# Optimization experiments

Hardware: AMD Instinct MI355X
Metric: run time of the kernel (lower is better)

## Reference

```python
import jax, jax.numpy as jnp
import numpy as np

B, T, D = 4096, 200, 64
N_USERS, N_ITEMS = 100000, 100000


def _linear_init(k, out_dim, in_dim):
    kw, kb = jax.random.split(k)
    lim = 1.0 / np.sqrt(in_dim)
    w = jax.random.uniform(kw, (out_dim, in_dim), minval=-lim, maxval=lim, dtype=jnp.float32)
    b = jax.random.uniform(kb, (out_dim,), minval=-lim, maxval=lim, dtype=jnp.float32)
    return w, b


def setup_inputs() -> dict:
    key = jax.random.key(0)
    ks = jax.random.split(key, 16)
    gru_w_ih, gru_b_ih = _linear_init(ks[0], 3 * D, D)   # torch GRU gate order: r, z, n
    gru_w_hh, gru_b_hh = _linear_init(ks[1], 3 * D, D)
    attn_w, attn_b = _linear_init(ks[2], D, D)
    wr_w, wr_b = _linear_init(ks[3], D, 2 * D)
    wz_w, wz_b = _linear_init(ks[4], D, 2 * D)
    wh_w, wh_b = _linear_init(ks[5], D, 2 * D)
    aux_w, aux_b = _linear_init(ks[6], 1, D)
    item_emb = jax.random.normal(ks[7], (N_ITEMS + 1, D), dtype=jnp.float32)
    user_bias = jax.random.normal(ks[8], (N_USERS, 1), dtype=jnp.float32) * 0.01
    item_bias = jax.random.normal(ks[9], (N_ITEMS, 1), dtype=jnp.float32) * 0.01
    u_idx = jax.random.randint(ks[10], (B,), 0, N_USERS)
    i_idx = jax.random.randint(ks[11], (B,), 0, N_ITEMS)
    seq = jax.random.randint(ks[12], (B, T), 0, N_ITEMS + 1)
    return dict(u_idx=u_idx, i_idx=i_idx, seq=seq,
                item_emb=item_emb, user_bias=user_bias, item_bias=item_bias,
                gru_w_ih=gru_w_ih, gru_b_ih=gru_b_ih, gru_w_hh=gru_w_hh, gru_b_hh=gru_b_hh,
                attn_w=attn_w, attn_b=attn_b,
                wr_w=wr_w, wr_b=wr_b, wz_w=wz_w, wz_b=wz_b, wh_w=wh_w, wh_b=wh_b,
                aux_w=aux_w, aux_b=aux_b)


def _gru(seq_emb, w_ih, b_ih, w_hh, b_hh):
    # seq_emb: [B, T, D]. Precompute input projections for all timesteps.
    x_proj = jnp.einsum('btd,gd->btg', seq_emb, w_ih) + b_ih  # [B, T, 3D]
    x_proj = jnp.transpose(x_proj, (1, 0, 2))                 # [T, B, 3D]
    h0 = jnp.zeros((seq_emb.shape[0], D), dtype=seq_emb.dtype)

    def step(h, xp):
        gh = h @ w_hh.T + b_hh
        xr, xz, xn = jnp.split(xp, 3, axis=-1)
        hr, hz, hn = jnp.split(gh, 3, axis=-1)
        r = jax.nn.sigmoid(xr + hr)
        z = jax.nn.sigmoid(xz + hz)
        n = jnp.tanh(xn + r * hn)
        h_new = (1.0 - z) * n + z * h
        return h_new, h_new

    _, hs = jax.lax.scan(step, h0, x_proj)
    return jnp.transpose(hs, (1, 0, 2))  # [B, T, D]


def _augru(seq_emb, attn_w_t, wr_w, wr_b, wz_w, wz_b, wh_w, wh_b):
    # Split each [D, 2D] weight into x-part and h-part (input was concat([x, h])).
    wr_x, wr_h = wr_w[:, :D], wr_w[:, D:]
    wz_x, wz_h = wz_w[:, :D], wz_w[:, D:]
    wh_x, wh_h = wh_w[:, :D], wh_w[:, D:]
    xr = jnp.einsum('btd,hd->bth', seq_emb, wr_x) + wr_b  # [B, T, D]
    xz = jnp.einsum('btd,hd->bth', seq_emb, wz_x) + wz_b
    xh = jnp.einsum('btd,hd->bth', seq_emb, wh_x) + wh_b
    h0 = jnp.zeros((seq_emb.shape[0], D), dtype=seq_emb.dtype)
    inputs = (jnp.transpose(xr, (1, 0, 2)), jnp.transpose(xz, (1, 0, 2)),
              jnp.transpose(xh, (1, 0, 2)), attn_w_t.T)  # [T,B,D]x3, [T,B]

    def step(h, inp):
        xr_t, xz_t, xh_t, a_t = inp
        r = jax.nn.sigmoid(xr_t + h @ wr_h.T)
        z = jax.nn.sigmoid(xz_t + h @ wz_h.T)
        h_hat = jnp.tanh(xh_t + (r * h) @ wh_h.T)
        z = a_t[:, None] * z
        h_new = (1.0 - z) * h + z * h_hat
        return h_new, None

    h_final, _ = jax.lax.scan(step, h0, inputs)
    return h_final  # [B, D]


def reference(u_idx, i_idx, seq, item_emb, user_bias, item_bias,
              gru_w_ih, gru_b_ih, gru_w_hh, gru_b_hh, attn_w, attn_b,
              wr_w, wr_b, wz_w, wz_b, wh_w, wh_b, aux_w, aux_b):
    fm1 = user_bias[u_idx] + item_bias[i_idx]          # [B, 1]
    target_emb = item_emb[i_idx]                       # [B, D]
    seq_emb = item_emb[seq]                            # [B, T, D]

    gru_out = _gru(seq_emb, gru_w_ih, gru_b_ih, gru_w_hh, gru_b_hh)  # [B, T, D]

    target_proj = target_emb @ attn_w.T + attn_b       # [B, D]
    attn_scores = jnp.einsum('btd,bd->bt', gru_out, target_proj)
    attn_weights = jax.nn.sigmoid(attn_scores)         # [B, T]

    attn_vec = _augru(seq_emb, attn_weights, wr_w, wr_b, wz_w, wz_b, wh_w, wh_b)  # [B, D]

    aux_logits = (gru_out[:, -1, :] @ aux_w.T + aux_b)[:, 0]  # [B]
    return (fm1, attn_vec, aux_logits)
```

## Files before the change

kernel.cpp:

```cpp
#include <hip/hip_runtime.h>

typedef __bf16 bf16x8 __attribute__((ext_vector_type(8)));
typedef float f32x4 __attribute__((ext_vector_type(4)));

#define T_LEN 200
#define NB 4096

__device__ __forceinline__ f32x4 mfma16(bf16x8 a, bf16x8 b, f32x4 c) {
    return __builtin_amdgcn_mfma_f32_16x16x32_bf16(a, b, c, 0, 0, 0);
}
__device__ __forceinline__ float sigf(float x) {
    return __builtin_amdgcn_rcpf(1.0f + __expf(-x));
}
__device__ __forceinline__ float tanh_fast(float x) {
    return 1.0f - 2.0f * __builtin_amdgcn_rcpf(__expf(2.0f * x) + 1.0f);
}

__device__ __forceinline__ unsigned packRNE2(float a, float b) {
    unsigned ha = (unsigned)__builtin_bit_cast(unsigned short, (__bf16)a);
    unsigned hb = (unsigned)__builtin_bit_cast(unsigned short, (__bf16)b);
    return ha | (hb << 16);
}
__device__ __forceinline__ void publish_hi(unsigned short* hp, float v) {
    __bf16 h = (__bf16)v;
    *hp = __builtin_bit_cast(unsigned short, h);
}

struct Frag { bf16x8 hi, lo; };
__device__ __forceinline__ Frag make_frag(f32x4 a, f32x4 b) {
    Frag f;
    #pragma unroll
    for (int j = 0; j < 4; j++) {
        float v = a[j]; __bf16 h = (__bf16)v;
        f.hi[j] = h; f.lo[j] = (__bf16)(v - (float)h);
    }
    #pragma unroll
    for (int j = 0; j < 4; j++) {
        float v = b[j]; __bf16 h = (__bf16)v;
        f.hi[4 + j] = h; f.lo[4 + j] = (__bf16)(v - (float)h);
    }
    return f;
}
__device__ __forceinline__ bf16x8 load_w(const float* p) {
    f32x4 a = *(const f32x4*)p, b = *(const f32x4*)(p + 4);
    bf16x8 w;
    #pragma unroll
    for (int j = 0; j < 4; j++) { w[j] = (__bf16)a[j]; w[4 + j] = (__bf16)b[j]; }
    return w;
}

__global__ __launch_bounds__(512, 2)
void dien_fused(const int* __restrict__ u_idx, const int* __restrict__ i_idx,
                const int* __restrict__ seq, const float* __restrict__ item_emb,
                const float* __restrict__ user_bias, const float* __restrict__ item_bias,
                const float* __restrict__ gw_ih, const float* __restrict__ gb_ih,
                const float* __restrict__ gw_hh, const float* __restrict__ gb_hh,
                const float* __restrict__ attn_w, const float* __restrict__ attn_b,
                const float* __restrict__ wr_w, const float* __restrict__ wr_b,
                const float* __restrict__ wz_w, const float* __restrict__ wz_b,
                const float* __restrict__ wh_w, const float* __restrict__ wh_b,
                const float* __restrict__ aux_w, const float* __restrict__ aux_b,
                float* __restrict__ out)
{
    __shared__ int sSeq[16][T_LEN];
    __shared__ __align__(16) float sTP[16][64];
    __shared__ __align__(16) unsigned short sHGhi[16][72];
    __shared__ __align__(16) unsigned short sHAhi[16][72];
    __shared__ __align__(16) unsigned short sRHhi[16][72];
    __shared__ __align__(16) unsigned short sXhi[16][72];
    __shared__ float sScore[2][16];
    __shared__ float sParts[16][4];

    const int tid  = threadIdx.x;
    const int wave = tid >> 6;
    const int lane = tid & 63;
    const int c    = lane & 15;
    const int q    = lane >> 4;
    const bool isG = (wave < 4);
    const int wg   = wave & 3;
    const int dglob = wg * 16 + c;
    const int row0 = blockIdx.x * 16;

    for (int i = tid; i < 16 * T_LEN; i += 512) {
        int b = i / T_LEN, t = i - b * T_LEN;
        sSeq[b][t] = seq[(row0 + b) * T_LEN + t];
    }

    if (tid < 16) {
        int b = row0 + tid;
        out[b] = user_bias[u_idx[b]] + item_bias[i_idx[b]];
    }

    if (tid < 256) {
        int b  = tid >> 4;
        int d0 = (tid & 15) * 4;
        const float* erow = item_emb + (long)i_idx[row0 + b] * 64;
        float e[64];
        #pragma unroll
        for (int k4 = 0; k4 < 16; k4++) {
            f32x4 v = *(const f32x4*)(erow + k4 * 4);
            #pragma unroll
            for (int j = 0; j < 4; j++) e[k4 * 4 + j] = v[j];
        }
        #pragma unroll
        for (int dd = 0; dd < 4; dd++) {
            int d = d0 + dd;
            const float* wrow = attn_w + d * 64;
            float s = attn_b[d];
            #pragma unroll
            for (int k4 = 0; k4 < 16; k4++) {
                f32x4 wv = *(const f32x4*)(wrow + k4 * 4);
                #pragma unroll
                for (int j = 0; j < 4; j++) s += e[k4 * 4 + j] * wv[j];
            }
            sTP[b][d] = s;
        }
    }

    for (int i = tid; i < 16 * 72; i += 512) sHAhi[0][i] = 0;
    const int xrow = wg * 4 + (lane >> 4);
    const int xch  = lane & 15;
    if (isG) {
        const float* p = item_emb + (long)seq[(row0 + xrow) * T_LEN + 0] * 64 + xch * 4;
        f32x4 v = *(const f32x4*)p;
        *(uint2*)&sXhi[xrow][xch * 4] =
            make_uint2(packRNE2(v[0], v[1]), packRNE2(v[2], v[3]));
    }
    __syncthreads();

    bf16x8 W[12];
    if (isG) {
        #pragma unroll
        for (int g = 0; g < 3; g++)
            #pragma unroll
            for (int s = 0; s < 2; s++) {
                W[g * 2 + s]     = load_w(gw_ih + (g * 64 + dglob) * 64 + s * 32 + q * 8);
                W[6 + g * 2 + s] = load_w(gw_hh + (g * 64 + dglob) * 64 + s * 32 + q * 8);
            }
    } else {
        #pragma unroll
        for (int s = 0; s < 2; s++) {
            const int fo = dglob * 128 + s * 32 + q * 8;
            W[0 + s]  = load_w(wr_w + fo);
            W[2 + s]  = load_w(wr_w + fo + 64);
            W[4 + s]  = load_w(wz_w + fo);
            W[6 + s]  = load_w(wz_w + fo + 64);
            W[8 + s]  = load_w(wh_w + fo);
            W[10 + s] = load_w(wh_w + fo + 64);
        }
    }

    float bA, bB, bC, bD;
    if (isG) {
        bA = gb_ih[dglob] + gb_hh[dglob];
        bB = gb_ih[64 + dglob] + gb_hh[64 + dglob];
        bC = gb_ih[128 + dglob];
        bD = gb_hh[128 + dglob];
    } else {
        bA = wr_b[dglob];
        bB = wz_b[dglob];
        bC = wh_b[dglob];
        bD = 0.0f;
    }
    const float auxwc = aux_w[dglob];

    Frag tpB0, tpB1;
    if (isG) {
        tpB0 = make_frag(*(const f32x4*)&sTP[c][q * 8], *(const f32x4*)&sTP[c][q * 8 + 4]);
        tpB1 = make_frag(*(const f32x4*)&sTP[c][32 + q * 8], *(const f32x4*)&sTP[c][32 + q * 8 + 4]);
    }

    float hst[4] = {0.f, 0.f, 0.f, 0.f};
    bf16x8 fr0, fr1;
    #pragma unroll
    for (int j = 0; j < 8; j++) { fr0[j] = (__bf16)0.f; fr1[j] = (__bf16)0.f; }
    f32x4 aAH = {0.f, 0.f, 0.f, 0.f};
    float z_c[4] = {0.f, 0.f, 0.f, 0.f};

    for (int t = 0; t < T_LEN; t++) {
        f32x4 xg;
        f32x4 aAR, aAZ;

        bf16x8 x0 = *(const bf16x8*)&sXhi[c][q * 8];
        bf16x8 x1 = *(const bf16x8*)&sXhi[c][32 + q * 8];

        if (isG) {
            int tn = (t + 1 < T_LEN) ? t + 1 : t;
            xg = *(const f32x4*)(item_emb + (long)sSeq[xrow][tn] * 64 + xch * 4);

            f32x4 accR = {bA, bA, bA, bA};
            accR = mfma16(x0, W[0], accR); accR = mfma16(x1, W[1], accR);
            accR = mfma16(fr0, W[6], accR); accR = mfma16(fr1, W[7], accR);
            f32x4 accZ = {bB, bB, bB, bB};
            accZ = mfma16(x0, W[2], accZ); accZ = mfma16(x1, W[3], accZ);
            accZ = mfma16(fr0, W[8], accZ); accZ = mfma16(fr1, W[9], accZ);
            f32x4 accNX = {bC, bC, bC, bC};
            accNX = mfma16(x0, W[4], accNX); accNX = mfma16(x1, W[5], accNX);
            f32x4 accNH = {bD, bD, bD, bD};
            accNH = mfma16(fr0, W[10], accNH); accNH = mfma16(fr1, W[11], accNH);

            #pragma unroll
            for (int i = 0; i < 4; i++) {
                float r = sigf(accR[i]);
                float z = sigf(accZ[i]);
                float n = tanh_fast(accNX[i] + r * accNH[i]);
                float hn = n + z * (hst[i] - n);
                hst[i] = hn;
                publish_hi(&sHGhi[q * 4 + i][dglob], hn);
            }
        } else {
            if (t > 0) {
                bf16x8 rh0 = *(const bf16x8*)&sRHhi[c][q * 8];
                bf16x8 rh1 = *(const bf16x8*)&sRHhi[c][32 + q * 8];
                aAH = mfma16(rh0, W[10], aAH); aAH = mfma16(rh1, W[11], aAH);
                #pragma unroll
                for (int i = 0; i < 4; i++) {
                    int rr = q * 4 + i;
                    float a = sScore[(t - 1) & 1][rr];
                    float hh = tanh_fast(aAH[i]);
                    float zz = a * z_c[i];
                    float hv = hst[i] + zz * (hh - hst[i]);
                    hst[i] = hv;
                    publish_hi(&sHAhi[rr][dglob], hv);
                }
            }
            aAR = (f32x4){bA, bA, bA, bA};
            aAR = mfma16(x0, W[0], aAR); aAR = mfma16(x1, W[1], aAR);
            aAZ = (f32x4){bB, bB, bB, bB};
            aAZ = mfma16(x0, W[4], aAZ); aAZ = mfma16(x1, W[5], aAZ);
            aAH = (f32x4){bC, bC, bC, bC};
            aAH = mfma16(x0, W[8], aAH); aAH = mfma16(x1, W[9], aAH);
        }

        __syncthreads();

        if (isG) {
            fr0 = *(const bf16x8*)&sHGhi[c][q * 8];
            fr1 = *(const bf16x8*)&sHGhi[c][32 + q * 8];
            f32x4 sc = {0.f, 0.f, 0.f, 0.f};
            sc = mfma16(fr0, tpB0.hi, sc); sc = mfma16(fr0, tpB0.lo, sc);
            sc = mfma16(fr1, tpB1.hi, sc); sc = mfma16(fr1, tpB1.lo, sc);
            if (wg == 0 && (c >> 2) == q) {
                int i = c & 3;
                float d = (i == 0) ? sc[0] : (i == 1) ? sc[1] : (i == 2) ? sc[2] : sc[3];
                sScore[t & 1][c] = sigf(d);
            }
            *(uint2*)&sXhi[xrow][xch * 4] =
                make_uint2(packRNE2(xg[0], xg[1]), packRNE2(xg[2], xg[3]));
        } else {
            bf16x8 ha0 = *(const bf16x8*)&sHAhi[c][q * 8];
            bf16x8 ha1 = *(const bf16x8*)&sHAhi[c][32 + q * 8];
            aAR = mfma16(ha0, W[2], aAR); aAR = mfma16(ha1, W[3], aAR);
            aAZ = mfma16(ha0, W[6], aAZ); aAZ = mfma16(ha1, W[7], aAZ);
            #pragma unroll
            for (int i = 0; i < 4; i++) {
                float r = sigf(aAR[i]);
                z_c[i]  = sigf(aAZ[i]);
                float rh = r * hst[i];
                publish_hi(&sRHhi[q * 4 + i][dglob], rh);
            }
        }

        __syncthreads();
    }

    if (!isG) {
        bf16x8 rh0 = *(const bf16x8*)&sRHhi[c][q * 8];
        bf16x8 rh1 = *(const bf16x8*)&sRHhi[c][32 + q * 8];
        aAH = mfma16(rh0, W[10], aAH); aAH = mfma16(rh1, W[11], aAH);
        #pragma unroll
        for (int i = 0; i < 4; i++) {
            int rr = q * 4 + i;
            float a = sScore[(T_LEN - 1) & 1][rr];
            float hh = tanh_fast(aAH[i]);
            float zz = a * z_c[i];
            float hv = hst[i] + zz * (hh - hst[i]);
            out[NB + (row0 + rr) * 64 + dglob] = hv;
        }
    }

    if (isG) {
        float pa[4];
        #pragma unroll
        for (int i = 0; i < 4; i++) pa[i] = hst[i] * auxwc;
        #pragma unroll
        for (int m = 1; m < 16; m <<= 1) {
            #pragma unroll
            for (int i = 0; i < 4; i++) pa[i] += __shfl_xor(pa[i], m, 64);
        }
        if (c == 0) {
            #pragma unroll
            for (int i = 0; i < 4; i++) sParts[q * 4 + i][wg] = pa[i];
        }
    }
    __syncthreads();
    if (tid < 16) {
        out[NB + NB * 64 + row0 + tid] =
            sParts[tid][0] + sParts[tid][1] + sParts[tid][2] + sParts[tid][3] + aux_b[0];
    }
}

extern "C" void kernel_launch(void* const* d_in, const int* in_sizes, int n_in,
                              void* d_out, int out_size, void* d_ws, size_t ws_size,
                              hipStream_t stream) {
    dien_fused<<<dim3(256), dim3(512), 0, stream>>>(
        (const int*)d_in[0],
        (const int*)d_in[1],
        (const int*)d_in[2],
        (const float*)d_in[3],
        (const float*)d_in[4],
        (const float*)d_in[5],
        (const float*)d_in[6],
        (const float*)d_in[7],
        (const float*)d_in[8],
        (const float*)d_in[9],
        (const float*)d_in[10],
        (const float*)d_in[11],
        (const float*)d_in[12],
        (const float*)d_in[13],
        (const float*)d_in[14],
        (const float*)d_in[15],
        (const float*)d_in[16],
        (const float*)d_in[17],
        (const float*)d_in[18],
        (const float*)d_in[19],
        (float*)d_out);
}
```

Before: 264.9 us.

## Double-buffer staged sequence embeddings and prefetch two steps ahead in recurrent loop

The shared bf16 buffer of input embeddings becomes double-buffered. The global gather for the next timestep is issued two steps ahead, and x fragments are loaded right after the mid-step barrier instead of at the top of the loop. In the AUGRU waves, the input-projection MFMAs for the next step are reordered to run before the dependent hidden-state update, which gives the scheduler independent work to hide latency. The cost is extra shared memory and registers, which could hurt occupancy at 512 threads with two blocks per CU.

```diff
diff --git a/kernel.cpp b/kernel.cpp
--- a/kernel.cpp
+++ b/kernel.cpp
@@ -67,7 +67,7 @@
     __shared__ __align__(16) unsigned short sHGhi[16][72];
     __shared__ __align__(16) unsigned short sHAhi[16][72];
     __shared__ __align__(16) unsigned short sRHhi[16][72];
-    __shared__ __align__(16) unsigned short sXhi[16][72];
+    __shared__ __align__(16) unsigned short sXhi[2][16][72];
     __shared__ float sScore[2][16];
     __shared__ float sParts[16][4];
 
@@ -123,7 +123,7 @@
     if (isG) {
         const float* p = item_emb + (long)seq[(row0 + xrow) * T_LEN + 0] * 64 + xch * 4;
         f32x4 v = *(const f32x4*)p;
-        *(uint2*)&sXhi[xrow][xch * 4] =
+        *(uint2*)&sXhi[0][xrow][xch * 4] =
             make_uint2(packRNE2(v[0], v[1]), packRNE2(v[2], v[3]));
     }
     __syncthreads();
@@ -162,6 +162,10 @@
         bC = wh_b[dglob];
         bD = 0.0f;
     }
+    const f32x4 vbA = {bA, bA, bA, bA};
+    const f32x4 vbB = {bB, bB, bB, bB};
+    const f32x4 vbC = {bC, bC, bC, bC};
+    const f32x4 vbD = {bD, bD, bD, bD};
     const float auxwc = aux_w[dglob];
 
     Frag tpB0, tpB1;
@@ -174,29 +178,33 @@
     bf16x8 fr0, fr1;
     #pragma unroll
     for (int j = 0; j < 8; j++) { fr0[j] = (__bf16)0.f; fr1[j] = (__bf16)0.f; }
-    f32x4 aAH = {0.f, 0.f, 0.f, 0.f};
+    f32x4 aAR = vbA, aAZ = vbB, aAH = vbC;
     float z_c[4] = {0.f, 0.f, 0.f, 0.f};
 
+    bf16x8 x0 = *(const bf16x8*)&sXhi[0][c][q * 8];
+    bf16x8 x1 = *(const bf16x8*)&sXhi[0][c][32 + q * 8];
+    f32x4 xg = {0.f, 0.f, 0.f, 0.f};
+    if (isG) {
+        int t1 = (1 < T_LEN) ? 1 : 0;
+        xg = *(const f32x4*)(item_emb + (long)sSeq[xrow][t1] * 64 + xch * 4);
+    }
+
     for (int t = 0; t < T_LEN; t++) {
-        f32x4 xg;
-        f32x4 aAR, aAZ;
-
-        bf16x8 x0 = *(const bf16x8*)&sXhi[c][q * 8];
-        bf16x8 x1 = *(const bf16x8*)&sXhi[c][32 + q * 8];
-
         if (isG) {
-            int tn = (t + 1 < T_LEN) ? t + 1 : t;
+            *(uint2*)&sXhi[(t + 1) & 1][xrow][xch * 4] =
+                make_uint2(packRNE2(xg[0], xg[1]), packRNE2(xg[2], xg[3]));
+            int tn = (t + 2 < T_LEN) ? t + 2 : T_LEN - 1;
             xg = *(const f32x4*)(item_emb + (long)sSeq[xrow][tn] * 64 + xch * 4);
 
-            f32x4 accR = {bA, bA, bA, bA};
+            f32x4 accR = vbA;
             accR = mfma16(x0, W[0], accR); accR = mfma16(x1, W[1], accR);
             accR = mfma16(fr0, W[6], accR); accR = mfma16(fr1, W[7], accR);
-            f32x4 accZ = {bB, bB, bB, bB};
+            f32x4 accZ = vbB;
             accZ = mfma16(x0, W[2], accZ); accZ = mfma16(x1, W[3], accZ);
             accZ = mfma16(fr0, W[8], accZ); accZ = mfma16(fr1, W[9], accZ);
-            f32x4 accNX = {bC, bC, bC, bC};
+            f32x4 accNX = vbC;
             accNX = mfma16(x0, W[4], accNX); accNX = mfma16(x1, W[5], accNX);
-            f32x4 accNH = {bD, bD, bD, bD};
+            f32x4 accNH = vbD;
             accNH = mfma16(fr0, W[10], accNH); accNH = mfma16(fr1, W[11], accNH);
 
             #pragma unroll
@@ -209,9 +217,18 @@
                 publish_hi(&sHGhi[q * 4 + i][dglob], hn);
             }
         } else {
+            bf16x8 rh0, rh1;
             if (t > 0) {
-                bf16x8 rh0 = *(const bf16x8*)&sRHhi[c][q * 8];
-                bf16x8 rh1 = *(const bf16x8*)&sRHhi[c][32 + q * 8];
+                rh0 = *(const bf16x8*)&sRHhi[c][q * 8];
+                rh1 = *(const bf16x8*)&sRHhi[c][32 + q * 8];
+            }
+            f32x4 nAR = vbA;
+            nAR = mfma16(x0, W[0], nAR); nAR = mfma16(x1, W[1], nAR);
+            f32x4 nAZ = vbB;
+            nAZ = mfma16(x0, W[4], nAZ); nAZ = mfma16(x1, W[5], nAZ);
+            f32x4 nAH = vbC;
+            nAH = mfma16(x0, W[8], nAH); nAH = mfma16(x1, W[9], nAH);
+            if (t > 0) {
                 aAH = mfma16(rh0, W[10], aAH); aAH = mfma16(rh1, W[11], aAH);
                 #pragma unroll
                 for (int i = 0; i < 4; i++) {
@@ -224,12 +241,7 @@
                     publish_hi(&sHAhi[rr][dglob], hv);
                 }
             }
-            aAR = (f32x4){bA, bA, bA, bA};
-            aAR = mfma16(x0, W[0], aAR); aAR = mfma16(x1, W[1], aAR);
-            aAZ = (f32x4){bB, bB, bB, bB};
-            aAZ = mfma16(x0, W[4], aAZ); aAZ = mfma16(x1, W[5], aAZ);
-            aAH = (f32x4){bC, bC, bC, bC};
-            aAH = mfma16(x0, W[8], aAH); aAH = mfma16(x1, W[9], aAH);
+            aAR = nAR; aAZ = nAZ; aAH = nAH;
         }
 
         __syncthreads();
@@ -237,6 +249,8 @@
         if (isG) {
             fr0 = *(const bf16x8*)&sHGhi[c][q * 8];
             fr1 = *(const bf16x8*)&sHGhi[c][32 + q * 8];
+            x0 = *(const bf16x8*)&sXhi[(t + 1) & 1][c][q * 8];
+            x1 = *(const bf16x8*)&sXhi[(t + 1) & 1][c][32 + q * 8];
             f32x4 sc = {0.f, 0.f, 0.f, 0.f};
             sc = mfma16(fr0, tpB0.hi, sc); sc = mfma16(fr0, tpB0.lo, sc);
             sc = mfma16(fr1, tpB1.hi, sc); sc = mfma16(fr1, tpB1.lo, sc);
@@ -245,11 +259,11 @@
                 float d = (i == 0) ? sc[0] : (i == 1) ? sc[1] : (i == 2) ? sc[2] : sc[3];
                 sScore[t & 1][c] = sigf(d);
             }
-            *(uint2*)&sXhi[xrow][xch * 4] =
-                make_uint2(packRNE2(xg[0], xg[1]), packRNE2(xg[2], xg[3]));
         } else {
             bf16x8 ha0 = *(const bf16x8*)&sHAhi[c][q * 8];
             bf16x8 ha1 = *(const bf16x8*)&sHAhi[c][32 + q * 8];
+            x0 = *(const bf16x8*)&sXhi[(t + 1) & 1][c][q * 8];
+            x1 = *(const bf16x8*)&sXhi[(t + 1) & 1][c][32 + q * 8];
             aAR = mfma16(ha0, W[2], aAR); aAR = mfma16(ha1, W[3], aAR);
             aAZ = mfma16(ha0, W[6], aAZ); aAZ = mfma16(ha1, W[7], aAZ);
             #pragma unroll
```

Result: slower. 289.4 us (+9.2%).
